# Performance work log

Measured on AMD Instinct MI355X. Metric: run time of the kernel, lower is better.

## Reference

```python
import jax, jax.numpy as jnp
import numpy as np

N_NODES = 100000
N_EDGES = 6400000
EPS = 1e-12


def _gcn_conv(x, edge_index, W, b, n):
    # PyG GCNConv(normalize=True): add self-loops, symmetric deg^-1/2 norm
    src, dst = edge_index[0], edge_index[1]
    loop = jnp.arange(n)
    row = jnp.concatenate([src, loop])
    col = jnp.concatenate([dst, loop])
    deg = jax.ops.segment_sum(jnp.ones(row.shape[0], dtype=x.dtype), col, num_segments=n)
    dinv = jnp.where(deg > 0, jax.lax.rsqrt(deg), 0.0)
    norm = dinv[row] * dinv[col]                       # [E+N]
    xw = x @ W                                          # [N,16]
    out = jax.ops.segment_sum(xw[row] * norm[:, None], col, num_segments=n)
    return out + b


def _sage_conv(x, edge_index, Wl, bl, Wr, n):
    # PyG SAGEConv(aggr='mean', root_weight=True, normalize=True)
    src, dst = edge_index[0], edge_index[1]
    deg = jax.ops.segment_sum(jnp.ones(src.shape[0], dtype=x.dtype), dst, num_segments=n)
    agg = jax.ops.segment_sum(x[src], dst, num_segments=n) / jnp.maximum(deg, 1.0)[:, None]
    out = agg @ Wl + bl + x @ Wr
    nrm = jnp.sqrt(jnp.sum(out * out, axis=-1, keepdims=True))
    return out / jnp.maximum(nrm, EPS)                  # F.normalize(p=2)


def setup_inputs() -> dict:
    key = jax.random.key(0)
    ks = jax.random.split(key, 16)
    s16, s128 = 1.0 / np.sqrt(16.0), 1.0 / np.sqrt(128.0)
    inp = {
        "x": jax.random.normal(ks[0], (N_NODES, 16), dtype=jnp.float32),
        "edge_index": jax.random.randint(ks[1], (2, N_EDGES), 0, N_NODES, dtype=jnp.int64),
        "W_gcn": jax.random.uniform(ks[2], (16, 16), jnp.float32, -s16, s16),
        "b_gcn": jnp.zeros((16,), jnp.float32),
        "Wl1": jax.random.uniform(ks[3], (16, 16), jnp.float32, -s16, s16),
        "bl1": jnp.zeros((16,), jnp.float32),
        "Wr1": jax.random.uniform(ks[4], (16, 16), jnp.float32, -s16, s16),
        "Wl2": jax.random.uniform(ks[5], (16, 16), jnp.float32, -s16, s16),
        "bl2": jnp.zeros((16,), jnp.float32),
        "Wr2": jax.random.uniform(ks[6], (16, 16), jnp.float32, -s16, s16),
        "W1": jax.random.uniform(ks[7], (16, 128), jnp.float32, -s16, s16),
        "b1": jax.random.uniform(ks[8], (128,), jnp.float32, -s16, s16),
        "W2": jax.random.uniform(ks[9], (128, 128), jnp.float32, -s128, s128),
        "b2": jax.random.uniform(ks[10], (128,), jnp.float32, -s128, s128),
        "W3": jax.random.uniform(ks[11], (128, 1), jnp.float32, -s128, s128),
        "b3": jax.random.uniform(ks[12], (1,), jnp.float32, -s128, s128),
    }
    return inp


def reference(x, edge_index, W_gcn, b_gcn, Wl1, bl1, Wr1, Wl2, bl2, Wr2, W1, b1, W2, b2, W3, b3):
    n = x.shape[0]
    h = jnp.tanh(_gcn_conv(x, edge_index, W_gcn, b_gcn, n))
    h = jnp.tanh(_sage_conv(h, edge_index, Wl1, bl1, Wr1, n))
    h = _sage_conv(h, edge_index, Wl2, bl2, Wr2, n)
    h = jax.nn.relu(h @ W1 + b1)
    h = jax.nn.relu(h @ W2 + b2)
    return h @ W3 + b3
```

## Files before the change

kernel.cpp:

```cpp
#include <hip/hip_runtime.h>
#include <hip/hip_bf16.h>
#include <math.h>

#define NBLK 512
#define ROWS (NBLK / 256)
#define MAXNC 512
#define STAGE_CAP 12512

__global__ void k_hist(const int* __restrict__ dst, int* __restrict__ hist,
                       int nE, int nc, int chunk) {
    __shared__ int ch[MAXNC];
    int b = blockIdx.x, t = threadIdx.x;
    for (int i = t; i < nc; i += 256) ch[i] = 0;
    __syncthreads();
    int c0 = b * chunk, c1 = min(nE, c0 + chunk);
    if (c1 > c0) {
        int nv = (c1 - c0) >> 2;
        const int4* d4 = (const int4*)(dst + c0);
        for (int i = t; i < nv; i += 256) {
            int4 dd = d4[i];
            atomicAdd(&ch[dd.x >> 8], 1);
            atomicAdd(&ch[dd.y >> 8], 1);
            atomicAdd(&ch[dd.z >> 8], 1);
            atomicAdd(&ch[dd.w >> 8], 1);
        }
        int rem = (c1 - c0) & 3;
        if (t < rem) atomicAdd(&ch[dst[c0 + (nv << 2) + t] >> 8], 1);
    }
    __syncthreads();
    for (int i = t; i < nc; i += 256) hist[b * nc + i] = ch[i];
}

__global__ void k_scanA(const int* __restrict__ hist, int* __restrict__ offT,
                        int* __restrict__ totPad, int* __restrict__ totReal, int nc) {
    __shared__ int sums[256];
    __shared__ int red[256];
    int c = blockIdx.x, t = threadIdx.x;
    int v[ROWS], p[ROWS];
    int s = 0, sr = 0;
#pragma unroll
    for (int j = 0; j < ROWS; ++j) {
        v[j] = hist[(size_t)(t * ROWS + j) * nc + c];
        p[j] = (v[j] + 15) & ~15;
        s += p[j];
        sr += v[j];
    }
    sums[t] = s;
    red[t] = sr;
    __syncthreads();
    for (int d = 1; d < 256; d <<= 1) {
        int x = (t >= d) ? sums[t - d] : 0;
        __syncthreads();
        sums[t] += x;
        __syncthreads();
    }
    int run = sums[t] - s;
#pragma unroll
    for (int j = 0; j < ROWS; ++j) {
        offT[(size_t)c * NBLK + t * ROWS + j] = run;
        run += p[j];
    }
    if (t == 255) totPad[c] = sums[255];
    for (int d = 128; d > 0; d >>= 1) {
        if (t < d) red[t] += red[t + d];
        __syncthreads();
    }
    if (t == 0) totReal[c] = red[0];
}

__global__ void k_scanB(const int* __restrict__ totPad, const int* __restrict__ totReal,
                        int* __restrict__ cbase, int* __restrict__ rbase,
                        int* __restrict__ rowstart, int nE, int nc, int n) {
    __shared__ int sp[512];
    __shared__ int sr[512];
    int t = threadIdx.x;
    int vp = (t < nc) ? totPad[t] : 0;
    int vr = (t < nc) ? totReal[t] : 0;
    sp[t] = vp; sr[t] = vr;
    __syncthreads();
    for (int d = 1; d < 512; d <<= 1) {
        int xp = (t >= d) ? sp[t - d] : 0;
        int xr = (t >= d) ? sr[t - d] : 0;
        __syncthreads();
        sp[t] += xp; sr[t] += xr;
        __syncthreads();
    }
    if (t < nc) { cbase[t] = sp[t] - vp; rbase[t] = sr[t] - vr; }
    if (t == nc - 1) cbase[nc] = sp[t];
    if (t == 0) rowstart[n] = nE;
}

__global__ __launch_bounds__(256, 2)
void k_fill(const int* __restrict__ src, const int* __restrict__ dst,
            const int* __restrict__ hist, const int* __restrict__ offT,
            const int* __restrict__ cbase,
            int* __restrict__ bucketed, int nE, int nc, int chunk) {
    __shared__ int stage[STAGE_CAP];
    __shared__ int sc[256];
    __shared__ int lbeg[MAXNC];
    __shared__ int lcur[MAXNC];
    int b = blockIdx.x, t = threadIdx.x;

    int v0 = (2 * t < nc) ? hist[(size_t)b * nc + 2 * t] : 0;
    int v1 = (2 * t + 1 < nc) ? hist[(size_t)b * nc + 2 * t + 1] : 0;
    int s = v0 + v1;
    sc[t] = s;
    __syncthreads();
    for (int d = 1; d < 256; d <<= 1) {
        int x = (t >= d) ? sc[t - d] : 0;
        __syncthreads();
        sc[t] += x;
        __syncthreads();
    }
    int excl = sc[t] - s;
    if (2 * t < nc) { lbeg[2 * t] = excl; lcur[2 * t] = excl; }
    if (2 * t + 1 < nc) { lbeg[2 * t + 1] = excl + v0; lcur[2 * t + 1] = excl + v0; }
    __syncthreads();

    int c0 = b * chunk, c1 = min(nE, c0 + chunk);
    if (c1 > c0) {
        int nv = (c1 - c0) >> 2;
        const int4* d4 = (const int4*)(dst + c0);
        const int4* s4 = (const int4*)(src + c0);
        for (int i = t; i < nv; i += 256) {
            int4 dd = d4[i];
            int4 ss = s4[i];
            int pos;
            pos = atomicAdd(&lcur[dd.x >> 8], 1); stage[pos] = ss.x | ((dd.x & 255) << 17);
            pos = atomicAdd(&lcur[dd.y >> 8], 1); stage[pos] = ss.y | ((dd.y & 255) << 17);
            pos = atomicAdd(&lcur[dd.z >> 8], 1); stage[pos] = ss.z | ((dd.z & 255) << 17);
            pos = atomicAdd(&lcur[dd.w >> 8], 1); stage[pos] = ss.w | ((dd.w & 255) << 17);
        }
        int rem = (c1 - c0) & 3;
        if (t < rem) {
            int e = c0 + (nv << 2) + t;
            int d = dst[e];
            int pos = atomicAdd(&lcur[d >> 8], 1);
            stage[pos] = src[e] | ((d & 255) << 17);
        }
    }
    __syncthreads();

    for (int c = t; c < nc; c += 256) {
        int lo = lbeg[c];
        int cnt = lcur[c] - lo;
        int g = cbase[c] + offT[(size_t)c * NBLK + b];
        int padded = (cnt + 15) & ~15;
        for (int i = 0; i < padded; i += 4) {
            int4 v;
            v.x = (i + 0 < cnt) ? stage[lo + i + 0] : -1;
            v.y = (i + 1 < cnt) ? stage[lo + i + 1] : -1;
            v.z = (i + 2 < cnt) ? stage[lo + i + 2] : -1;
            v.w = (i + 3 < cnt) ? stage[lo + i + 3] : -1;
            *(int4*)(bucketed + g + i) = v;
        }
    }
}

__global__ void k_fine(const int* __restrict__ bucketed, const int* __restrict__ cbase,
                       const int* __restrict__ rbase,
                       int* __restrict__ csr, int* __restrict__ rowstart,
                       float* __restrict__ dinv, int n) {
    __shared__ int cnt[256];
    __shared__ int lrs[512];
    __shared__ int cur[256];
    int cb = blockIdx.x, t = threadIdx.x;
    int e0 = cbase[cb], e1 = cbase[cb + 1];
    int r0 = rbase[cb];
    if (t < 256) cnt[t] = 0;
    __syncthreads();
    int nv = (e1 - e0) >> 2;
    const int4* b4 = (const int4*)(bucketed + e0);
    for (int i = t; i < nv; i += 512) {
        int4 en = b4[i];
        if (en.x >= 0) atomicAdd(&cnt[(en.x >> 17) & 255], 1);
        if (en.y >= 0) atomicAdd(&cnt[(en.y >> 17) & 255], 1);
        if (en.z >= 0) atomicAdd(&cnt[(en.z >> 17) & 255], 1);
        if (en.w >= 0) atomicAdd(&cnt[(en.w >> 17) & 255], 1);
    }
    __syncthreads();
    int my = (t < 256) ? cnt[t] : 0;
    lrs[t] = my;
    __syncthreads();
    for (int d = 1; d < 512; d <<= 1) {
        int x = (t >= d) ? lrs[t - d] : 0;
        __syncthreads();
        lrs[t] += x;
        __syncthreads();
    }
    if (t < 256) {
        int excl = lrs[t] - my;
        int node = cb * 256 + t;
        if (node < n) {
            rowstart[node] = r0 + excl;
            dinv[node] = rsqrtf((float)(my + 1));
        }
        cur[t] = r0 + excl;
    }
    __syncthreads();
    for (int i = t; i < nv; i += 512) {
        int4 en = b4[i];
        int pos;
        if (en.x >= 0) { pos = atomicAdd(&cur[(en.x >> 17) & 255], 1); csr[pos] = en.x & 0x1FFFF; }
        if (en.y >= 0) { pos = atomicAdd(&cur[(en.y >> 17) & 255], 1); csr[pos] = en.y & 0x1FFFF; }
        if (en.z >= 0) { pos = atomicAdd(&cur[(en.z >> 17) & 255], 1); csr[pos] = en.z & 0x1FFFF; }
        if (en.w >= 0) { pos = atomicAdd(&cur[(en.w >> 17) & 255], 1); csr[pos] = en.w & 0x1FFFF; }
    }
}

__global__ void k_prescale(const float* __restrict__ x, const float* __restrict__ dinv,
                           float* __restrict__ xs, int n) {
    int i = blockIdx.x * blockDim.x + threadIdx.x;
    if (i >= n) return;
    float di = dinv[i];
    const float4* xp = (const float4*)(x + (size_t)i * 16);
    float4* op = (float4*)(xs + (size_t)i * 16);
#pragma unroll
    for (int q = 0; q < 4; ++q) {
        float4 v = xp[q];
        v.x *= di; v.y *= di; v.z *= di; v.w *= di;
        op[q] = v;
    }
}

__global__ void k_agg(const float* __restrict__ hin, const int* __restrict__ csr,
                      const int* __restrict__ rowstart, float* __restrict__ agg, int n) {
    int wid = (blockIdx.x * blockDim.x + threadIdx.x) >> 6;
    if (wid >= n) return;
    int lane = threadIdx.x & 63;
    int q = lane >> 2;
    int c = lane & 3;
    int r0 = rowstart[wid], r1 = rowstart[wid + 1];
    int cnt = r1 - r0;
    const int* p = csr + r0 + q;
    int my = (cnt > q) ? ((cnt - q + 15) >> 4) : 0;
    const float4* hb = (const float4*)hin + c;

    float av[4] = {0.f, 0.f, 0.f, 0.f};
    int t = 0;
    for (; t + 4 <= my; t += 4) {
        int s0 = p[(t + 0) * 16];
        int s1 = p[(t + 1) * 16];
        int s2 = p[(t + 2) * 16];
        int s3 = p[(t + 3) * 16];
        float4 v0 = hb[(size_t)s0 * 4];
        float4 v1 = hb[(size_t)s1 * 4];
        float4 v2 = hb[(size_t)s2 * 4];
        float4 v3 = hb[(size_t)s3 * 4];
        av[0] += (v0.x + v1.x) + (v2.x + v3.x);
        av[1] += (v0.y + v1.y) + (v2.y + v3.y);
        av[2] += (v0.z + v1.z) + (v2.z + v3.z);
        av[3] += (v0.w + v1.w) + (v2.w + v3.w);
    }
    if (t + 2 <= my) {
        int s0 = p[(t + 0) * 16];
        int s1 = p[(t + 1) * 16];
        float4 v0 = hb[(size_t)s0 * 4];
        float4 v1 = hb[(size_t)s1 * 4];
        av[0] += v0.x + v1.x; av[1] += v0.y + v1.y;
        av[2] += v0.z + v1.z; av[3] += v0.w + v1.w;
        t += 2;
    }
    if (t < my) {
        int s0 = p[t * 16];
        float4 v0 = hb[(size_t)s0 * 4];
        av[0] += v0.x; av[1] += v0.y; av[2] += v0.z; av[3] += v0.w;
    }
#pragma unroll
    for (int m = 4; m <= 32; m <<= 1) {
#pragma unroll
        for (int j = 0; j < 4; ++j) av[j] += __shfl_xor(av[j], m);
    }
    if (q == 0)
        *(float4*)(agg + (size_t)wid * 16 + c * 4) = make_float4(av[0], av[1], av[2], av[3]);
}

template <int MODE>
__global__ void k_post(const float* __restrict__ agg, const float* __restrict__ hin,
                       const int* __restrict__ rowstart, const float* __restrict__ dinv,
                       const float* __restrict__ Wa, const float* __restrict__ ba,
                       const float* __restrict__ Wb,
                       float* __restrict__ hout, int n) {
    int idx = blockIdx.x * blockDim.x + threadIdx.x;
    int node = idx >> 2;
    if (node >= n) return;
    int t4 = idx & 3;
    int lane = threadIdx.x & 63;
    int lbase = lane & 60;

    float4 av = *(const float4*)(agg + (size_t)node * 16 + t4 * 4);
    float4 sv = *(const float4*)(hin + (size_t)node * 16 + t4 * 4);

    float a[16], s[16];
#pragma unroll
    for (int g = 0; g < 4; ++g) {
        a[g * 4 + 0] = __shfl(av.x, lbase + g);
        a[g * 4 + 1] = __shfl(av.y, lbase + g);
        a[g * 4 + 2] = __shfl(av.z, lbase + g);
        a[g * 4 + 3] = __shfl(av.w, lbase + g);
        s[g * 4 + 0] = __shfl(sv.x, lbase + g);
        s[g * 4 + 1] = __shfl(sv.y, lbase + g);
        s[g * 4 + 2] = __shfl(sv.z, lbase + g);
        s[g * 4 + 3] = __shfl(sv.w, lbase + g);
    }

    int fo = t4 * 4;
    float yv[4];
    if (MODE == 0) {
        float di = dinv[node];
#pragma unroll
        for (int k = 0; k < 16; ++k) a[k] = di * (a[k] + s[k]);
#pragma unroll
        for (int j = 0; j < 4; ++j) yv[j] = ba[fo + j];
#pragma unroll
        for (int k = 0; k < 16; ++k) {
            float4 w = *(const float4*)(Wa + k * 16 + fo);
            yv[0] += a[k] * w.x; yv[1] += a[k] * w.y;
            yv[2] += a[k] * w.z; yv[3] += a[k] * w.w;
        }
#pragma unroll
        for (int j = 0; j < 4; ++j) yv[j] = tanhf(yv[j]);
    } else {
        int cnt = rowstart[node + 1] - rowstart[node];
        float inv = 1.0f / fmaxf((float)cnt, 1.0f);
#pragma unroll
        for (int k = 0; k < 16; ++k) a[k] *= inv;
#pragma unroll
        for (int j = 0; j < 4; ++j) yv[j] = ba[fo + j];
#pragma unroll
        for (int k = 0; k < 16; ++k) {
            float4 wa = *(const float4*)(Wa + k * 16 + fo);
            float4 wb = *(const float4*)(Wb + k * 16 + fo);
            yv[0] += a[k] * wa.x + s[k] * wb.x;
            yv[1] += a[k] * wa.y + s[k] * wb.y;
            yv[2] += a[k] * wa.z + s[k] * wb.z;
            yv[3] += a[k] * wa.w + s[k] * wb.w;
        }
        float sq = yv[0] * yv[0] + yv[1] * yv[1] + yv[2] * yv[2] + yv[3] * yv[3];
        sq += __shfl_xor(sq, 1);
        sq += __shfl_xor(sq, 2);
        float nrm = fmaxf(sqrtf(sq), 1e-12f);
#pragma unroll
        for (int j = 0; j < 4; ++j) yv[j] /= nrm;
        if (MODE == 1) {
#pragma unroll
            for (int j = 0; j < 4; ++j) yv[j] = tanhf(yv[j]);
        }
    }
    *(float4*)(hout + (size_t)node * 16 + fo) = make_float4(yv[0], yv[1], yv[2], yv[3]);
}

#define MLP_NODES 64
__global__ __launch_bounds__(256)
void k_mlp(const float* __restrict__ h3,
           const float* __restrict__ W1, const float* __restrict__ b1,
           const float* __restrict__ W2, const float* __restrict__ b2,
           const float* __restrict__ W3, const float* __restrict__ b3,
           float* __restrict__ out, int n) {
    __shared__ float t1T[128][65];
    __shared__ float hpart[MLP_NODES][5];

    int t = threadIdx.x;
    int w = t >> 6;
    int l = t & 63;
    int ow = __builtin_amdgcn_readfirstlane(w * 32);
    int node0 = blockIdx.x * MLP_NODES;
    int node = node0 + l;
    int nodec = min(node, n - 1);

    float acc[32];
    {
        float h[16];
        const float4* hp = (const float4*)(h3 + (size_t)nodec * 16);
#pragma unroll
        for (int q = 0; q < 4; ++q) {
            float4 v = hp[q];
            h[q * 4 + 0] = v.x; h[q * 4 + 1] = v.y; h[q * 4 + 2] = v.z; h[q * 4 + 3] = v.w;
        }
        const float* bp = b1 + ow;
#pragma unroll
        for (int j = 0; j < 32; ++j) acc[j] = bp[j];
#pragma unroll
        for (int k = 0; k < 16; ++k) {
            const float* wr = W1 + k * 128 + ow;
            float hk = h[k];
#pragma unroll
            for (int j = 0; j < 32; ++j) acc[j] += hk * wr[j];
        }
#pragma unroll
        for (int j = 0; j < 32; ++j) t1T[ow + j][l] = fmaxf(acc[j], 0.f);
    }
    __syncthreads();

    {
        const float* bp = b2 + ow;
#pragma unroll
        for (int j = 0; j < 32; ++j) acc[j] = bp[j];
    }
    for (int k = 0; k < 128; ++k) {
        float tk = t1T[k][l];
        const float* wr = W2 + k * 128 + ow;
#pragma unroll
        for (int j = 0; j < 32; ++j) acc[j] += tk * wr[j];
    }

    float part = 0.f;
    {
        const float* wr = W3 + ow;
#pragma unroll
        for (int j = 0; j < 32; ++j) part += fmaxf(acc[j], 0.f) * wr[j];
    }
    hpart[l][w] = part;
    __syncthreads();
    if (w == 0 && node < n) {
        out[node] = hpart[l][0] + hpart[l][1] + hpart[l][2] + hpart[l][3] + b3[0];
    }
}

extern "C" void kernel_launch(void* const* d_in, const int* in_sizes, int n_in,
                              void* d_out, int out_size, void* d_ws, size_t ws_size,
                              hipStream_t stream) {
    const float* x = (const float*)d_in[0];
    const int* ei = (const int*)d_in[1];
    const float* W_gcn = (const float*)d_in[2];
    const float* b_gcn = (const float*)d_in[3];
    const float* Wl1 = (const float*)d_in[4];
    const float* bl1 = (const float*)d_in[5];
    const float* Wr1 = (const float*)d_in[6];
    const float* Wl2 = (const float*)d_in[7];
    const float* bl2 = (const float*)d_in[8];
    const float* Wr2 = (const float*)d_in[9];
    const float* W1 = (const float*)d_in[10];
    const float* b1 = (const float*)d_in[11];
    const float* W2 = (const float*)d_in[12];
    const float* b2 = (const float*)d_in[13];
    const float* W3 = (const float*)d_in[14];
    const float* b3 = (const float*)d_in[15];

    const int N = in_sizes[0] / 16;
    const int E = in_sizes[1] / 2;
    const int NC = (N + 255) >> 8;
    const int chunk = (((E + NBLK - 1) / NBLK) + 3) & ~3;
    const int* src = ei;
    const int* dst = ei + E;

    char* w = (char*)d_ws;
    auto alloc = [&](size_t bytes) {
        void* p = (void*)w;
        w += (bytes + 255) & ~(size_t)255;
        return p;
    };
    int* hist = (int*)alloc((size_t)NBLK * NC * 4);
    int* offT = (int*)alloc((size_t)NBLK * NC * 4);
    int* totPad = (int*)alloc((size_t)NC * 4);
    int* totReal = (int*)alloc((size_t)NC * 4);
    int* cbase = (int*)alloc((size_t)(NC + 1) * 4);
    int* rbase = (int*)alloc((size_t)NC * 4);
    int* rowstart = (int*)alloc((size_t)(N + 1) * 4);
    float* dinv = (float*)alloc((size_t)N * 4);
    int* bucketed = (int*)alloc(((size_t)E + (size_t)NBLK * NC * 16) * 4);
    int* csr = (int*)alloc((size_t)E * 4);
    float* xs = (float*)alloc((size_t)N * 16 * 4);
    float* agg = (float*)alloc((size_t)N * 16 * 4);
    float* h1 = (float*)alloc((size_t)N * 16 * 4);
    float* h2 = (float*)alloc((size_t)N * 16 * 4);
    float* h3 = (float*)alloc((size_t)N * 16 * 4);

    k_hist<<<NBLK, 256, 0, stream>>>(dst, hist, E, NC, chunk);
    k_scanA<<<NC, 256, 0, stream>>>(hist, offT, totPad, totReal, NC);
    k_scanB<<<1, 512, 0, stream>>>(totPad, totReal, cbase, rbase, rowstart, E, NC, N);
    k_fill<<<NBLK, 256, 0, stream>>>(src, dst, hist, offT, cbase, bucketed, E, NC, chunk);
    k_fine<<<NC, 512, 0, stream>>>(bucketed, cbase, rbase, csr, rowstart, dinv, N);

    int blk = 256;
    int ngrid = (N + blk - 1) / blk;
    long long agg_threads = (long long)N * 64;
    int agrid = (int)((agg_threads + blk - 1) / blk);
    int pgrid = (int)(((long long)N * 4 + blk - 1) / blk);

    k_prescale<<<ngrid, blk, 0, stream>>>(x, dinv, xs, N);

    k_agg<<<agrid, blk, 0, stream>>>(xs, csr, rowstart, agg, N);
    k_post<0><<<pgrid, blk, 0, stream>>>(agg, xs, rowstart, dinv, W_gcn, b_gcn, W_gcn, h1, N);

    k_agg<<<agrid, blk, 0, stream>>>(h1, csr, rowstart, agg, N);
    k_post<1><<<pgrid, blk, 0, stream>>>(agg, h1, rowstart, dinv, Wl1, bl1, Wr1, h2, N);

    k_agg<<<agrid, blk, 0, stream>>>(h2, csr, rowstart, agg, N);
    k_post<2><<<pgrid, blk, 0, stream>>>(agg, h2, rowstart, dinv, Wl2, bl2, Wr2, h3, N);

    int mgrid = (N + MLP_NODES - 1) / MLP_NODES;
    k_mlp<<<mgrid, blk, 0, stream>>>(h3, W1, b1, W2, b2, W3, b3, (float*)d_out, N);
}
```

Before: 335.2 us.

## Split neighbor aggregation into two source-half passes and widen MLP tile

Edges of each CSR row are partitioned by whether the source index falls in the lower or upper half of the nodes. Aggregation then runs as two passes, each gathering from only half of the feature table, so the gathered working set is more likely to stay cache-resident. k_post sums the two partial results. The index loads and aggregate stores are made nontemporal, and the MLP kernel now processes 128 nodes per block so each W2 weight load is reused across two nodes. The price is twice the aggregation launches, an extra partial buffer and split array, and higher register and shared-memory pressure in the MLP (launch bounds now allow one block per SM).

```diff
diff --git a/kernel.cpp b/kernel.cpp
--- a/kernel.cpp
+++ b/kernel.cpp
@@ -6,6 +6,8 @@
 #define ROWS (NBLK / 256)
 #define MAXNC 512
 #define STAGE_CAP 12512
+
+typedef float vfloat4 __attribute__((ext_vector_type(4)));
 
 __global__ void k_hist(const int* __restrict__ dst, int* __restrict__ hist,
                        int nE, int nc, int chunk) {
@@ -160,26 +162,27 @@
 __global__ void k_fine(const int* __restrict__ bucketed, const int* __restrict__ cbase,
                        const int* __restrict__ rbase,
                        int* __restrict__ csr, int* __restrict__ rowstart,
-                       float* __restrict__ dinv, int n) {
-    __shared__ int cnt[256];
+                       int* __restrict__ split, float* __restrict__ dinv,
+                       int n, int half) {
+    __shared__ int cnt2[512];
     __shared__ int lrs[512];
-    __shared__ int cur[256];
+    __shared__ int cur[512];
     int cb = blockIdx.x, t = threadIdx.x;
     int e0 = cbase[cb], e1 = cbase[cb + 1];
     int r0 = rbase[cb];
-    if (t < 256) cnt[t] = 0;
+    cnt2[t] = 0;
     __syncthreads();
     int nv = (e1 - e0) >> 2;
     const int4* b4 = (const int4*)(bucketed + e0);
     for (int i = t; i < nv; i += 512) {
         int4 en = b4[i];
-        if (en.x >= 0) atomicAdd(&cnt[(en.x >> 17) & 255], 1);
-        if (en.y >= 0) atomicAdd(&cnt[(en.y >> 17) & 255], 1);
-        if (en.z >= 0) atomicAdd(&cnt[(en.z >> 17) & 255], 1);
-        if (en.w >= 0) atomicAdd(&cnt[(en.w >> 17) & 255], 1);
-    }
-    __syncthreads();
-    int my = (t < 256) ? cnt[t] : 0;
+        if (en.x >= 0) atomicAdd(&cnt2[(((en.x >> 17) & 255) << 1) | ((en.x & 0x1FFFF) >= half)], 1);
+        if (en.y >= 0) atomicAdd(&cnt2[(((en.y >> 17) & 255) << 1) | ((en.y & 0x1FFFF) >= half)], 1);
+        if (en.z >= 0) atomicAdd(&cnt2[(((en.z >> 17) & 255) << 1) | ((en.z & 0x1FFFF) >= half)], 1);
+        if (en.w >= 0) atomicAdd(&cnt2[(((en.w >> 17) & 255) << 1) | ((en.w & 0x1FFFF) >= half)], 1);
+    }
+    __syncthreads();
+    int my = cnt2[t];
     lrs[t] = my;
     __syncthreads();
     for (int d = 1; d < 512; d <<= 1) {
@@ -188,23 +191,24 @@
         lrs[t] += x;
         __syncthreads();
     }
-    if (t < 256) {
-        int excl = lrs[t] - my;
-        int node = cb * 256 + t;
+    cur[t] = r0 + (lrs[t] - my);
+    if ((t & 1) == 0) {
+        int node = cb * 256 + (t >> 1);
         if (node < n) {
-            rowstart[node] = r0 + excl;
-            dinv[node] = rsqrtf((float)(my + 1));
-        }
-        cur[t] = r0 + excl;
+            rowstart[node] = r0 + (lrs[t] - my);
+            split[node]    = r0 + lrs[t];
+            int deg = my + cnt2[t + 1];
+            dinv[node] = rsqrtf((float)(deg + 1));
+        }
     }
     __syncthreads();
     for (int i = t; i < nv; i += 512) {
         int4 en = b4[i];
-        int pos;
-        if (en.x >= 0) { pos = atomicAdd(&cur[(en.x >> 17) & 255], 1); csr[pos] = en.x & 0x1FFFF; }
-        if (en.y >= 0) { pos = atomicAdd(&cur[(en.y >> 17) & 255], 1); csr[pos] = en.y & 0x1FFFF; }
-        if (en.z >= 0) { pos = atomicAdd(&cur[(en.z >> 17) & 255], 1); csr[pos] = en.z & 0x1FFFF; }
-        if (en.w >= 0) { pos = atomicAdd(&cur[(en.w >> 17) & 255], 1); csr[pos] = en.w & 0x1FFFF; }
+        int s, pos;
+        if (en.x >= 0) { s = en.x & 0x1FFFF; pos = atomicAdd(&cur[(((en.x >> 17) & 255) << 1) | (s >= half)], 1); csr[pos] = s; }
+        if (en.y >= 0) { s = en.y & 0x1FFFF; pos = atomicAdd(&cur[(((en.y >> 17) & 255) << 1) | (s >= half)], 1); csr[pos] = s; }
+        if (en.z >= 0) { s = en.z & 0x1FFFF; pos = atomicAdd(&cur[(((en.z >> 17) & 255) << 1) | (s >= half)], 1); csr[pos] = s; }
+        if (en.w >= 0) { s = en.w & 0x1FFFF; pos = atomicAdd(&cur[(((en.w >> 17) & 255) << 1) | (s >= half)], 1); csr[pos] = s; }
     }
 }
 
@@ -224,13 +228,14 @@
 }
 
 __global__ void k_agg(const float* __restrict__ hin, const int* __restrict__ csr,
-                      const int* __restrict__ rowstart, float* __restrict__ agg, int n) {
+                      const int* __restrict__ lo, const int* __restrict__ hi,
+                      float* __restrict__ agg, int n) {
     int wid = (blockIdx.x * blockDim.x + threadIdx.x) >> 6;
     if (wid >= n) return;
     int lane = threadIdx.x & 63;
     int q = lane >> 2;
     int c = lane & 3;
-    int r0 = rowstart[wid], r1 = rowstart[wid + 1];
+    int r0 = lo[wid], r1 = hi[wid];
     int cnt = r1 - r0;
     const int* p = csr + r0 + q;
     int my = (cnt > q) ? ((cnt - q + 15) >> 4) : 0;
@@ -239,10 +244,10 @@
     float av[4] = {0.f, 0.f, 0.f, 0.f};
     int t = 0;
     for (; t + 4 <= my; t += 4) {
-        int s0 = p[(t + 0) * 16];
-        int s1 = p[(t + 1) * 16];
-        int s2 = p[(t + 2) * 16];
-        int s3 = p[(t + 3) * 16];
+        int s0 = __builtin_nontemporal_load(p + (t + 0) * 16);
+        int s1 = __builtin_nontemporal_load(p + (t + 1) * 16);
+        int s2 = __builtin_nontemporal_load(p + (t + 2) * 16);
+        int s3 = __builtin_nontemporal_load(p + (t + 3) * 16);
         float4 v0 = hb[(size_t)s0 * 4];
         float4 v1 = hb[(size_t)s1 * 4];
         float4 v2 = hb[(size_t)s2 * 4];
@@ -253,8 +258,8 @@
         av[3] += (v0.w + v1.w) + (v2.w + v3.w);
     }
     if (t + 2 <= my) {
-        int s0 = p[(t + 0) * 16];
-        int s1 = p[(t + 1) * 16];
+        int s0 = __builtin_nontemporal_load(p + (t + 0) * 16);
+        int s1 = __builtin_nontemporal_load(p + (t + 1) * 16);
         float4 v0 = hb[(size_t)s0 * 4];
         float4 v1 = hb[(size_t)s1 * 4];
         av[0] += v0.x + v1.x; av[1] += v0.y + v1.y;
@@ -262,7 +267,7 @@
         t += 2;
     }
     if (t < my) {
-        int s0 = p[t * 16];
+        int s0 = __builtin_nontemporal_load(p + t * 16);
         float4 v0 = hb[(size_t)s0 * 4];
         av[0] += v0.x; av[1] += v0.y; av[2] += v0.z; av[3] += v0.w;
     }
@@ -271,12 +276,15 @@
 #pragma unroll
         for (int j = 0; j < 4; ++j) av[j] += __shfl_xor(av[j], m);
     }
-    if (q == 0)
-        *(float4*)(agg + (size_t)wid * 16 + c * 4) = make_float4(av[0], av[1], av[2], av[3]);
+    if (q == 0) {
+        vfloat4 o = {av[0], av[1], av[2], av[3]};
+        __builtin_nontemporal_store(o, (vfloat4*)(agg + (size_t)wid * 16 + c * 4));
+    }
 }
 
 template <int MODE>
-__global__ void k_post(const float* __restrict__ agg, const float* __restrict__ hin,
+__global__ void k_post(const float* __restrict__ aggA, const float* __restrict__ aggB,
+                       const float* __restrict__ hin,
                        const int* __restrict__ rowstart, const float* __restrict__ dinv,
                        const float* __restrict__ Wa, const float* __restrict__ ba,
                        const float* __restrict__ Wb,
@@ -288,8 +296,10 @@
     int lane = threadIdx.x & 63;
     int lbase = lane & 60;
 
-    float4 av = *(const float4*)(agg + (size_t)node * 16 + t4 * 4);
+    float4 aA = *(const float4*)(aggA + (size_t)node * 16 + t4 * 4);
+    float4 aB = *(const float4*)(aggB + (size_t)node * 16 + t4 * 4);
     float4 sv = *(const float4*)(hin + (size_t)node * 16 + t4 * 4);
+    float4 av = make_float4(aA.x + aB.x, aA.y + aB.y, aA.z + aB.z, aA.w + aB.w);
 
     float a[16], s[16];
 #pragma unroll
@@ -350,14 +360,14 @@
     *(float4*)(hout + (size_t)node * 16 + fo) = make_float4(yv[0], yv[1], yv[2], yv[3]);
 }
 
-#define MLP_NODES 64
-__global__ __launch_bounds__(256)
+#define MLP_NODES 128
+__global__ __launch_bounds__(256, 1)
 void k_mlp(const float* __restrict__ h3,
            const float* __restrict__ W1, const float* __restrict__ b1,
            const float* __restrict__ W2, const float* __restrict__ b2,
            const float* __restrict__ W3, const float* __restrict__ b3,
            float* __restrict__ out, int n) {
-    __shared__ float t1T[128][65];
+    __shared__ float t1T[128][130];
     __shared__ float hpart[MLP_NODES][5];
 
     int t = threadIdx.x;
@@ -365,18 +375,21 @@
     int l = t & 63;
     int ow = __builtin_amdgcn_readfirstlane(w * 32);
     int node0 = blockIdx.x * MLP_NODES;
-    int node = node0 + l;
-    int nodec = min(node, n - 1);
-
-    float acc[32];
-    {
+    int nA = min(node0 + l, n - 1);
+    int nB = min(node0 + 64 + l, n - 1);
+
+#pragma unroll
+    for (int half = 0; half < 2; ++half) {
+        int nd = half ? nB : nA;
+        int col = half * 64 + l;
         float h[16];
-        const float4* hp = (const float4*)(h3 + (size_t)nodec * 16);
+        const float4* hp = (const float4*)(h3 + (size_t)nd * 16);
 #pragma unroll
         for (int q = 0; q < 4; ++q) {
             float4 v = hp[q];
             h[q * 4 + 0] = v.x; h[q * 4 + 1] = v.y; h[q * 4 + 2] = v.z; h[q * 4 + 3] = v.w;
         }
+        float acc[32];
         const float* bp = b1 + ow;
 #pragma unroll
         for (int j = 0; j < 32; ++j) acc[j] = bp[j];
@@ -388,32 +401,45 @@
             for (int j = 0; j < 32; ++j) acc[j] += hk * wr[j];
         }
 #pragma unroll
-        for (int j = 0; j < 32; ++j) t1T[ow + j][l] = fmaxf(acc[j], 0.f);
-    }
-    __syncthreads();
-
+        for (int j = 0; j < 32; ++j) t1T[ow + j][col] = fmaxf(acc[j], 0.f);
+    }
+    __syncthreads();
+
+    float accA[32], accB[32];
     {
         const float* bp = b2 + ow;
 #pragma unroll
-        for (int j = 0; j < 32; ++j) acc[j] = bp[j];
+        for (int j = 0; j < 32; ++j) { accA[j] = bp[j]; accB[j] = bp[j]; }
     }
     for (int k = 0; k < 128; ++k) {
-        float tk = t1T[k][l];
+        float tkA = t1T[k][l];
+        float tkB = t1T[k][64 + l];
         const float* wr = W2 + k * 128 + ow;
 #pragma unroll
-        for (int j = 0; j < 32; ++j) acc[j] += tk * wr[j];
-    }
-
-    float part = 0.f;
+        for (int j = 0; j < 32; ++j) {
+            float wj = wr[j];
+            accA[j] += tkA * wj;
+            accB[j] += tkB * wj;
+        }
+    }
+
+    float pA = 0.f, pB = 0.f;
     {
         const float* wr = W3 + ow;
 #pragma unroll
-        for (int j = 0; j < 32; ++j) part += fmaxf(acc[j], 0.f) * wr[j];
-    }
-    hpart[l][w] = part;
-    __syncthreads();
-    if (w == 0 && node < n) {
-        out[node] = hpart[l][0] + hpart[l][1] + hpart[l][2] + hpart[l][3] + b3[0];
+        for (int j = 0; j < 32; ++j) {
+            float wj = wr[j];
+            pA += fmaxf(accA[j], 0.f) * wj;
+            pB += fmaxf(accB[j], 0.f) * wj;
+        }
+    }
+    hpart[l][w] = pA;
+    hpart[64 + l][w] = pB;
+    __syncthreads();
+    if (t < MLP_NODES) {
+        int node = node0 + t;
+        if (node < n)
+            out[node] = hpart[t][0] + hpart[t][1] + hpart[t][2] + hpart[t][3] + b3[0];
     }
 }
 
@@ -441,6 +467,7 @@
     const int E = in_sizes[1] / 2;
     const int NC = (N + 255) >> 8;
     const int chunk = (((E + NBLK - 1) / NBLK) + 3) & ~3;
+    const int half = (N + 1) >> 1;
     const int* src = ei;
     const int* dst = ei + E;
 
@@ -457,11 +484,13 @@
     int* cbase = (int*)alloc((size_t)(NC + 1) * 4);
     int* rbase = (int*)alloc((size_t)NC * 4);
     int* rowstart = (int*)alloc((size_t)(N + 1) * 4);
+    int* split = (int*)alloc((size_t)N * 4);
     float* dinv = (float*)alloc((size_t)N * 4);
     int* bucketed = (int*)alloc(((size_t)E + (size_t)NBLK * NC * 16) * 4);
     int* csr = (int*)alloc((size_t)E * 4);
     float* xs = (float*)alloc((size_t)N * 16 * 4);
-    float* agg = (float*)alloc((size_t)N * 16 * 4);
+    float* aggA = (float*)alloc((size_t)N * 16 * 4);
+    float* aggB = (float*)alloc((size_t)N * 16 * 4);
     float* h1 = (float*)alloc((size_t)N * 16 * 4);
     float* h2 = (float*)alloc((size_t)N * 16 * 4);
     float* h3 = (float*)alloc((size_t)N * 16 * 4);
@@ -470,7 +499,7 @@
     k_scanA<<<NC, 256, 0, stream>>>(hist, offT, totPad, totReal, NC);
     k_scanB<<<1, 512, 0, stream>>>(totPad, totReal, cbase, rbase, rowstart, E, NC, N);
     k_fill<<<NBLK, 256, 0, stream>>>(src, dst, hist, offT, cbase, bucketed, E, NC, chunk);
-    k_fine<<<NC, 512, 0, stream>>>(bucketed, cbase, rbase, csr, rowstart, dinv, N);
+    k_fine<<<NC, 512, 0, stream>>>(bucketed, cbase, rbase, csr, rowstart, split, dinv, N, half);
 
     int blk = 256;
     int ngrid = (N + blk - 1) / blk;
@@ -480,14 +509,15 @@
 
     k_prescale<<<ngrid, blk, 0, stream>>>(x, dinv, xs, N);
 
-    k_agg<<<agrid, blk, 0, stream>>>(xs, csr, rowstart, agg, N);
-    k_post<0><<<pgrid, blk, 0, stream>>>(agg, xs, rowstart, dinv, W_gcn, b_gcn, W_gcn, h1, N);
-
-    k_agg<<<agrid, blk, 0, stream>>>(h1, csr, rowstart, agg, N);
-    k_post<1><<<pgrid, blk, 0, stream>>>(agg, h1, rowstart, dinv, Wl1, bl1, Wr1, h2, N);
-
-    k_agg<<<agrid, blk, 0, stream>>>(h2, csr, rowstart, agg, N);
-    k_post<2><<<pgrid, blk, 0, stream>>>(agg, h2, rowstart, dinv, Wl2, bl2, Wr2, h3, N);
+    k_agg<<<agrid, blk, 0, stream>>>(xs, csr, rowstart, split, aggA, N);
+    k_agg<<<agrid, blk, 0, stream>>>(xs, csr, split, rowstart + 1, aggB, N);
+    k_post<0><<<pgrid, blk, 0, stream>>>(aggA, aggB, xs, rowstart, dinv, W_gcn, b_gcn, W_gcn, h1, N);
+    k_agg<<<agrid, blk, 0, stream>>>(h1, csr, rowstart, split, aggA, N);
+    k_agg<<<agrid, blk, 0, stream>>>(h1, csr, split, rowstart + 1, aggB, N);
+    k_post<1><<<pgrid, blk, 0, stream>>>(aggA, aggB, h1, rowstart, dinv, Wl1, bl1, Wr1, h2, N);
+    k_agg<<<agrid, blk, 0, stream>>>(h2, csr, rowstart, split, aggA, N);
+    k_agg<<<agrid, blk, 0, stream>>>(h2, csr, split, rowstart + 1, aggB, N);
+    k_post<2><<<pgrid, blk, 0, stream>>>(aggA, aggB, h2, rowstart, dinv, Wl2, bl2, Wr2, h3, N);
 
     int mgrid = (N + MLP_NODES - 1) / MLP_NODES;
     k_mlp<<<mgrid, blk, 0, stream>>>(h3, W1, b1, W2, b2, W3, b3, (float*)d_out, N);
```

After: 413.6 us. 23.4% more time.
